# Kernel tuning notes

Hardware: AMD Instinct MI355X
Metric: run time of the kernel (lower is better)

## Reference

```python
import jax, jax.numpy as jnp
import numpy as np
from jax import lax

C, H, W, N = 128, 48, 48, 16
SHIFT_W = 1   # frozen value of p_3_1_1 (random.randint(-3,3) in original)
SHIFT_C = 1   # frozen value of p_11_0_1


def setup_inputs() -> dict:
    key = jax.random.key(0)
    k1, k2, k3, k4, k5 = jax.random.split(key, 5)
    x = jax.random.normal(k1, (N, C, H, W), dtype=jnp.float32)
    # p_5_w: trunc_normal std=0.02, shape (1,c,h,w)
    p5_w = 0.02 * jax.random.truncated_normal(k2, -2.0, 2.0, (1, C, H, W), dtype=jnp.float32)
    # p_6: 1x1 conv c->c, no bias -> weight (c, c)
    w6 = jax.random.normal(k3, (C, C), dtype=jnp.float32) / np.float32(np.sqrt(C))
    # p_8: Conv2d(1, c//2, (1,5), dilation=(1,3), padding=(0,6), bias=False)
    w8 = jax.random.normal(k4, (C // 2, 1, 1, 5), dtype=jnp.float32) / np.float32(np.sqrt(5))
    # p_10: 1x1 conv 3c/2 -> c, no bias
    w10 = jax.random.normal(k5, (C, 3 * C // 2), dtype=jnp.float32) / np.float32(np.sqrt(3 * C // 2))
    return {"x": x, "p5_w": p5_w, "w6": w6, "w8": w8, "w10": w10}


def _forward(x, p5_w, w6, w8, w10):
    n, c, h, w = x.shape
    hw = h * w
    inv_sqrt_c = np.float32(1.0 / np.sqrt(c))
    inv_sqrt_hw = np.float32(1.0 / np.sqrt(hw))

    t1 = x.max(axis=1)                                    # (n,h,w) channel max
    t2 = -x
    t4 = jnp.maximum(t2, jnp.roll(t2, SHIFT_W, axis=3))    # roll along width
    t5 = p5_w * t4
    t6 = jnp.einsum('oc,nchw->nohw', w6, t5)               # 1x1 conv p_6

    # score tensor t_7: (n, hw, hw)
    t7 = jnp.einsum('ncp,ncq->npq', t6.reshape(n, c, hw), x.reshape(n, c, hw)) * inv_sqrt_c

    # dilated 1x5 conv on channel-max map
    t8 = lax.conv_general_dilated(
        t1[:, None, :, :], w8, window_strides=(1, 1),
        padding=((0, 0), (6, 6)), rhs_dilation=(1, 3),
        dimension_numbers=('NCHW', 'OIHW', 'NCHW'))        # (n, c/2, h, w)

    # unfold kernel (3,1), dilation (2,1), padding (2,0): rows i-2, i, i+2
    pad = jnp.pad(t8, ((0, 0), (0, 0), (2, 2), (0, 0)))
    t9 = jnp.stack([pad[:, :, 2 * k:2 * k + h, :] for k in range(3)], axis=2)  # (n,c/2,3,h,w)

    t10 = jnp.einsum('oc,nchw->nohw', w10, t9.reshape(n, 3 * c // 2, h, w))   # 1x1 conv p_10
    t11 = jnp.roll(t10, SHIFT_C, axis=1)                   # roll along channels
    t12 = jnp.maximum(x, t11)

    # out[n,q,c] = sum_p t7[n,p,q] * t12[n,c,p]
    t13 = jnp.einsum('npq,ncp->nqc', t7, t12.reshape(n, c, hw)) * inv_sqrt_hw
    return t13.reshape(n, h, w, c).transpose(0, 3, 1, 2)   # (n,c,h,w)


def reference(x, p5_w, w6, w8, w10):
    return _forward(x, p5_w, w6, w8, w10)
```

## Files before the change

kernel.cpp:

```cpp
#include <hip/hip_runtime.h>
#include <cmath>

typedef short bf16x8 __attribute__((ext_vector_type(8)));
typedef short bf16x4 __attribute__((ext_vector_type(4)));
typedef float f32x4 __attribute__((ext_vector_type(4)));

namespace {
constexpr int kN   = 16;
constexpr int kC   = 128;
constexpr int kH   = 48;
constexpr int kW   = 48;
constexpr int kHW  = kH * kW;
constexpr int kK9  = 192;
constexpr int kNPC = 18;
constexpr int kPCH = kHW / kNPC;
constexpr int kLS  = 132;
constexpr int kPA  = 136;
}

__device__ __forceinline__ unsigned short f2b(float f) {
  unsigned u = __builtin_bit_cast(unsigned, f);
  u = (u + 0x7FFFu + ((u >> 16) & 1u)) >> 16;
  return (unsigned short)u;
}
__device__ __forceinline__ float b2f(unsigned short u) {
  return __builtin_bit_cast(float, ((unsigned)u) << 16);
}

__device__ __forceinline__ int tidx(int w, int c) {
  return w * kLS + (c ^ (((w >> 2) & 3) << 3));
}

__global__ __launch_bounds__(256)
void k_prep(const float* __restrict__ p5, const float* __restrict__ w6,
            const float* __restrict__ w10, const float* __restrict__ w8,
            float* __restrict__ p5T, unsigned short* __restrict__ w6b,
            float* __restrict__ Weff) {
  const int tid = threadIdx.x;
  const int bb = blockIdx.x;
  if (bb < 48) {
    __shared__ float Ls[kW * kLS];
    const int h = bb;
    for (int i = 0; i < 6; ++i) {
      const int idx = i * 256 + tid;
      const int c = idx / 12, s = idx % 12;
      const float4 v = *(const float4*)(p5 + (size_t)c * kHW + h * kW + s * 4);
      const int sw = (s & 3) << 3;
      Ls[(4 * s + 0) * kLS + (c ^ sw)] = v.x;
      Ls[(4 * s + 1) * kLS + (c ^ sw)] = v.y;
      Ls[(4 * s + 2) * kLS + (c ^ sw)] = v.z;
      Ls[(4 * s + 3) * kLS + (c ^ sw)] = v.w;
    }
    __syncthreads();
    for (int i = 0; i < 3; ++i) {
      const int idx = i * 256 + tid;
      const int w = idx >> 4, c = (idx & 15) * 8;
      const float* s = &Ls[tidx(w, c)];
      float4 a{s[0], s[1], s[2], s[3]}, b{s[4], s[5], s[6], s[7]};
      float* dst = p5T + ((size_t)(h * kW + w)) * kC + c;
      *(float4*)dst = a;
      *(float4*)(dst + 4) = b;
    }
  } else if (bb < 112) {
    const int i = (bb - 48) * 256 + tid;
    w6b[i] = f2b(w6[i]);
  } else {
    const int idx = (bb - 112) * 256 + tid;
    if (idx < kC * 15) {
      const int o = idx / 15, t = idx - o * 15;
      const int kk = t / 5, j = t - kk * 5;
      float s = 0.f;
#pragma unroll
      for (int c2 = 0; c2 < 64; ++c2)
        s = fmaf(w10[o * kK9 + 3 * c2 + kk], w8[c2 * 5 + j], s);
      Weff[idx] = s;
    }
  }
}

__global__ __launch_bounds__(256)
void k_xt5t6(const float* __restrict__ x, const float* __restrict__ p5T,
             const unsigned short* __restrict__ w6b,
             unsigned short* __restrict__ xT, unsigned short* __restrict__ xB,
             float* __restrict__ t1, unsigned short* __restrict__ t6) {
  __shared__ __align__(16) float Ls[kW * kLS];
  __shared__ __align__(16) unsigned short w6s[kC * kPA];
  __shared__ __align__(16) unsigned short t5s[kW * kPA];
  const int b = blockIdx.x;
  const int n = b / kH, h = b - n * kH;
  const int tid = threadIdx.x;
  const float* xrow = x + (size_t)n * kC * kHW + h * kW;
  unsigned short* xBrow = xB + (size_t)n * kC * kHW + h * kW;
  for (int i = 0; i < 6; ++i) {
    const int idx = i * 256 + tid;
    const int c = idx / 12, s = idx % 12;
    const float4 v = *(const float4*)(xrow + (size_t)c * kHW + s * 4);
    const int sw = (s & 3) << 3;
    Ls[(4 * s + 0) * kLS + (c ^ sw)] = v.x;
    Ls[(4 * s + 1) * kLS + (c ^ sw)] = v.y;
    Ls[(4 * s + 2) * kLS + (c ^ sw)] = v.z;
    Ls[(4 * s + 3) * kLS + (c ^ sw)] = v.w;
    bf16x4 xb4{(short)f2b(v.x), (short)f2b(v.y), (short)f2b(v.z), (short)f2b(v.w)};
    *(bf16x4*)(xBrow + (size_t)c * kHW + s * 4) = xb4;
  }
  for (int i = 0; i < 8; ++i) {
    const int f = i * 256 + tid;
    const int o = f >> 4, seg = (f & 15) * 8;
    *(bf16x8*)&w6s[o * kPA + seg] = *(const bf16x8*)(w6b + o * kC + seg);
  }
  __syncthreads();

  for (int i = 0; i < 3; ++i) {
    const int idx = i * 256 + tid;
    const int w = idx >> 4, c = (idx & 15) * 8;
    const int wp = (w == 0) ? (kW - 1) : (w - 1);
    const float* sv = &Ls[tidx(w, c)];
    const float* sp = &Ls[tidx(wp, c)];
    const int q = h * kW + w;
    const float* pv = p5T + (size_t)q * kC + c;

    unsigned short xb[8], tb[8];
    float m = -3.4e38f;
#pragma unroll
    for (int j = 0; j < 8; ++j) {
      const float xv = sv[j];
      const float t5 = pv[j] * fmaxf(-xv, -sp[j]);
      xb[j] = f2b(xv);
      tb[j] = f2b(t5);
      m = fmaxf(m, xv);
    }
    *(bf16x8*)(xT + ((size_t)n * kHW + q) * kC + c) = *(const bf16x8*)xb;
    *(bf16x8*)&t5s[w * kPA + c] = *(const bf16x8*)tb;
#pragma unroll
    for (int off = 1; off < 16; off <<= 1)
      m = fmaxf(m, __shfl_xor(m, off, 16));
    if ((tid & 15) == 0) t1[(size_t)n * kHW + q] = m;
  }
  __syncthreads();

  const int wv = tid >> 6, lane = tid & 63;
  const int lr = lane & 15, lk = (lane >> 4) * 8;
  f32x4 acc[2][3];
#pragma unroll
  for (int i = 0; i < 2; ++i)
#pragma unroll
    for (int j = 0; j < 3; ++j) acc[i][j] = f32x4{0.f, 0.f, 0.f, 0.f};
#pragma unroll
  for (int ks = 0; ks < kC; ks += 32) {
    bf16x8 a[2], bf[3];
#pragma unroll
    for (int mt = 0; mt < 2; ++mt)
      a[mt] = *(const bf16x8*)&w6s[(32 * wv + 16 * mt + lr) * kPA + ks + lk];
#pragma unroll
    for (int nt = 0; nt < 3; ++nt)
      bf[nt] = *(const bf16x8*)&t5s[(16 * nt + lr) * kPA + ks + lk];
#pragma unroll
    for (int mt = 0; mt < 2; ++mt)
#pragma unroll
      for (int nt = 0; nt < 3; ++nt)
        acc[mt][nt] = __builtin_amdgcn_mfma_f32_16x16x32_bf16(a[mt], bf[nt], acc[mt][nt], 0, 0, 0);
  }
#pragma unroll
  for (int mt = 0; mt < 2; ++mt)
#pragma unroll
    for (int nt = 0; nt < 3; ++nt) {
      const int q = h * kW + 16 * nt + lr;
#pragma unroll
      for (int r = 0; r < 4; ++r) {
        const int o = 32 * wv + 16 * mt + 4 * (lane >> 4) + r;
        t6[((size_t)n * kC + o) * kHW + q] = f2b(acc[mt][nt][r]);
      }
    }
}

__global__ __launch_bounds__(256)
void k_corr(const unsigned short* __restrict__ xB, const float* __restrict__ t1,
            const float* __restrict__ Weff, const unsigned short* __restrict__ t6,
            unsigned short* __restrict__ part) {
  __shared__ __align__(16) unsigned short t12s[kC * kPA];
  __shared__ __align__(16) unsigned short Bsf[kC * kPA];
  __shared__ __align__(16) float t1s[8 * 60];
  __shared__ float sW[kC][15];
  const int tid = threadIdx.x;
  const int n = blockIdx.y;
  const int chunk = blockIdx.x;
  const int p0 = chunk * kPCH;
  const int h_lo = p0 / kW;
  const unsigned short* Bg = t6 + (size_t)n * kC * kHW + p0;

  for (int i = tid; i < 8 * 60; i += 256) {
    const int r = i / 60, cc = i - r * 60;
    const int hh = h_lo - 2 + r, ww = cc - 6;
    t1s[i] = (hh >= 0 && hh < kH && ww >= 0 && ww < kW) ? t1[n * kHW + hh * kW + ww] : 0.f;
  }
  for (int i = tid; i < kC * 15; i += 256) {
    const int c = i / 15, t = i - c * 15;
    sW[c][t] = Weff[((c - 1) & (kC - 1)) * 15 + t];
  }
#pragma unroll
  for (int i = 0; i < 8; ++i) {
    const int f = i * 256 + tid;
    const int c = f >> 4, seg = (f & 15) * 8;
    *(bf16x8*)&Bsf[c * kPA + seg] = *(const bf16x8*)(Bg + (size_t)c * kHW + seg);
  }
  __syncthreads();

  const unsigned short* xn = xB + (size_t)n * kC * kHW;
  for (int it = 0; it < 8; ++it) {
    const int idx = it * 256 + tid;
    const int c = idx >> 4, p = (idx & 15) * 8;
    const int q = p0 + p;
    const int h = q / kW, w0 = q - h * kW;
    const int r0 = h - h_lo;
    float tap[3][20];
#pragma unroll
    for (int kk = 0; kk < 3; ++kk) {
      const float* src = &t1s[(r0 + 2 * kk) * 60 + w0];
#pragma unroll
      for (int j4 = 0; j4 < 5; ++j4) {
        const float4 v = *(const float4*)(src + 4 * j4);
        tap[kk][4 * j4 + 0] = v.x; tap[kk][4 * j4 + 1] = v.y;
        tap[kk][4 * j4 + 2] = v.z; tap[kk][4 * j4 + 3] = v.w;
      }
    }
    float wr[15];
#pragma unroll
    for (int t = 0; t < 15; ++t) wr[t] = sW[c][t];
    const bf16x8 xv8 = *(const bf16x8*)(xn + (size_t)c * kHW + q);
    unsigned short o16[8];
#pragma unroll
    for (int dp = 0; dp < 8; ++dp) {
      float acc = 0.f;
#pragma unroll
      for (int kk = 0; kk < 3; ++kk)
#pragma unroll
        for (int j = 0; j < 5; ++j)
          acc = fmaf(wr[kk * 5 + j], tap[kk][3 * j + dp], acc);
      o16[dp] = f2b(fmaxf(b2f((unsigned short)xv8[dp]), acc));
    }
    *(bf16x8*)&t12s[c * kPA + p] = *(const bf16x8*)o16;
  }
  __syncthreads();

  const int wv = tid >> 6, lane = tid & 63;
  const int lr = lane & 15, lk = (lane >> 4) * 8;
  const int wr2 = (wv >> 1) * 64, wc2 = (wv & 1) * 64;
  f32x4 acc[4][4];
#pragma unroll
  for (int i = 0; i < 4; ++i)
#pragma unroll
    for (int j = 0; j < 4; ++j) acc[i][j] = f32x4{0.f, 0.f, 0.f, 0.f};

#pragma unroll
  for (int ks = 0; ks < kPCH; ks += 32) {
    bf16x8 a[4], bv[4];
#pragma unroll
    for (int i = 0; i < 4; ++i) {
      a[i]  = *(const bf16x8*)&t12s[(wr2 + 16 * i + lr) * kPA + ks + lk];
      bv[i] = *(const bf16x8*)&Bsf[(wc2 + 16 * i + lr) * kPA + ks + lk];
    }
#pragma unroll
    for (int i = 0; i < 4; ++i)
#pragma unroll
      for (int j = 0; j < 4; ++j)
        acc[i][j] = __builtin_amdgcn_mfma_f32_16x16x32_bf16(a[i], bv[j], acc[i][j], 0, 0, 0);
  }

  unsigned short* dst = part + ((size_t)chunk * kN + n) * (kC * kC);
#pragma unroll
  for (int i = 0; i < 4; ++i)
#pragma unroll
    for (int j = 0; j < 4; ++j)
#pragma unroll
      for (int r = 0; r < 4; ++r)
        dst[(wr2 + 16 * i + 4 * (lane >> 4) + r) * kC + wc2 + 16 * j + lr] = f2b(acc[i][j][r]);
}

__global__ __launch_bounds__(256)
void k_redM(const unsigned short* __restrict__ part, unsigned short* __restrict__ M) {
  const int bid = blockIdx.x;
  const int j = bid >> 4, n = bid & 15;
  const int r0 = (j * 256 + threadIdx.x) * 8;
  float acc[8];
#pragma unroll
  for (int e = 0; e < 8; ++e) acc[e] = 0.f;
#pragma unroll
  for (int ch = 0; ch < kNPC; ++ch) {
    const bf16x8 v = *(const bf16x8*)(part + (((size_t)ch * kN + n) << 14) + r0);
#pragma unroll
    for (int e = 0; e < 8; ++e) acc[e] += b2f((unsigned short)v[e]);
  }
  unsigned short o16[8];
#pragma unroll
  for (int e = 0; e < 8; ++e) o16[e] = f2b(acc[e]);
  *(bf16x8*)(M + ((size_t)n << 14) + r0) = *(const bf16x8*)o16;
}

__global__ __launch_bounds__(256)
void k_out(const unsigned short* __restrict__ A, const unsigned short* __restrict__ B,
           float* __restrict__ Out, float scale) {
  constexpr int K = 128;
  __shared__ __align__(16) unsigned short As[kC * kPA];
  __shared__ __align__(16) unsigned short Bs[64 * kPA];
  const int tid = threadIdx.x;
  const int n = blockIdx.y;
  const int qbase = blockIdx.x * 64;
  const unsigned short* Ag = A + (size_t)n * kC * K;
  const unsigned short* Bg = B + ((size_t)n * kHW + qbase) * K;

  {
    const int m = tid >> 1, hf = tid & 1;
    const unsigned short* src = Ag + (size_t)m * K + hf * 64;
    unsigned short* dst = &As[m * kPA + hf * 64];
#pragma unroll
    for (int i = 0; i < 8; ++i)
      *(bf16x8*)(dst + 8 * i) = *(const bf16x8*)(src + 8 * i);
  }
#pragma unroll
  for (int i = 0; i < 4; ++i) {
    const int f = i * 256 + tid;
    const int q = f >> 4, seg = (f & 15) * 8;
    *(bf16x8*)&Bs[q * kPA + seg] = *(const bf16x8*)(Bg + (size_t)q * K + seg);
  }
  __syncthreads();

  const int wv = tid >> 6, lane = tid & 63;
  const int lr = lane & 15, lk = (lane >> 4) * 8;

  f32x4 acc[2][4];
#pragma unroll
  for (int i = 0; i < 2; ++i)
#pragma unroll
    for (int j = 0; j < 4; ++j) acc[i][j] = f32x4{0.f, 0.f, 0.f, 0.f};

#pragma unroll
  for (int ks = 0; ks < K; ks += 32) {
    bf16x8 a[2], b[4];
#pragma unroll
    for (int mt = 0; mt < 2; ++mt)
      a[mt] = *(const bf16x8*)&As[(32 * wv + 16 * mt + lr) * kPA + ks + lk];
#pragma unroll
    for (int nt = 0; nt < 4; ++nt)
      b[nt] = *(const bf16x8*)&Bs[(16 * nt + lr) * kPA + ks + lk];
#pragma unroll
    for (int mt = 0; mt < 2; ++mt)
#pragma unroll
      for (int nt = 0; nt < 4; ++nt)
        acc[mt][nt] = __builtin_amdgcn_mfma_f32_16x16x32_bf16(
            a[mt], b[nt], acc[mt][nt], 0, 0, 0);
  }

#pragma unroll
  for (int mt = 0; mt < 2; ++mt)
#pragma unroll
    for (int nt = 0; nt < 4; ++nt) {
      const int q = qbase + 16 * nt + lr;
#pragma unroll
      for (int r = 0; r < 4; ++r) {
        const int m = 32 * wv + 16 * mt + 4 * (lane >> 4) + r;
        Out[((size_t)n * kC + m) * kHW + q] = scale * acc[mt][nt][r];
      }
    }
}

extern "C" void kernel_launch(void* const* d_in, const int* in_sizes, int n_in,
                              void* d_out, int out_size, void* d_ws, size_t ws_size,
                              hipStream_t stream) {
  const float* x   = (const float*)d_in[0];
  const float* p5  = (const float*)d_in[1];
  const float* w6  = (const float*)d_in[2];
  const float* w8  = (const float*)d_in[3];
  const float* w10 = (const float*)d_in[4];
  float* out = (float*)d_out;

  char* ws = (char*)d_ws;
  unsigned short* xT   = (unsigned short*)(ws);
  unsigned short* t6b  = (unsigned short*)(ws + 9437184);
  unsigned short* part = (unsigned short*)(ws + 18874368);
  unsigned short* xB   = (unsigned short*)(ws + 28311552);
  unsigned short* Mb   = (unsigned short*)(ws + 37748736);
  float*          t1b  = (float*)(ws + 38273024);
  unsigned short* w6b  = (unsigned short*)(ws + 38420480);
  float*          Weff = (float*)(ws + 38453248);
  float*          p5T  = (float*)(ws + 38460928);

  const float scale = 1.0f / (sqrtf((float)kC) * sqrtf((float)kHW));

  k_prep<<<120, 256, 0, stream>>>(p5, w6, w10, w8, p5T, w6b, Weff);
  k_xt5t6<<<kN * kH, 256, 0, stream>>>(x, p5T, w6b, xT, xB, t1b, t6b);
  k_corr<<<dim3(kNPC, kN), 256, 0, stream>>>(xB, t1b, Weff, t6b, part);
  k_redM<<<8 * kN, 256, 0, stream>>>(part, Mb);
  k_out<<<dim3(kHW / 64, kN), 256, 0, stream>>>(Mb, xT, out, scale);
}
```

Measured before the change: 48.71 us.

## Fuse partial reduction into k_corr via last-block atomic counter; drop LDS staging

```diff
diff --git a/kernel.cpp b/kernel.cpp
--- a/kernel.cpp
+++ b/kernel.cpp
@@ -35,7 +35,7 @@
 void k_prep(const float* __restrict__ p5, const float* __restrict__ w6,
             const float* __restrict__ w10, const float* __restrict__ w8,
             float* __restrict__ p5T, unsigned short* __restrict__ w6b,
-            float* __restrict__ Weff) {
+            float* __restrict__ Weff, int* __restrict__ cnt) {
   const int tid = threadIdx.x;
   const int bb = blockIdx.x;
   if (bb < 48) {
@@ -75,6 +75,7 @@
         s = fmaf(w10[o * kK9 + 3 * c2 + kk], w8[c2 * 5 + j], s);
       Weff[idx] = s;
     }
+    if (bb == 119 && tid < kN) cnt[tid] = 0;
   }
 }
 
@@ -84,7 +85,6 @@
              unsigned short* __restrict__ xT, unsigned short* __restrict__ xB,
              float* __restrict__ t1, unsigned short* __restrict__ t6) {
   __shared__ __align__(16) float Ls[kW * kLS];
-  __shared__ __align__(16) unsigned short w6s[kC * kPA];
   __shared__ __align__(16) unsigned short t5s[kW * kPA];
   const int b = blockIdx.x;
   const int n = b / kH, h = b - n * kH;
@@ -103,11 +103,6 @@
     bf16x4 xb4{(short)f2b(v.x), (short)f2b(v.y), (short)f2b(v.z), (short)f2b(v.w)};
     *(bf16x4*)(xBrow + (size_t)c * kHW + s * 4) = xb4;
   }
-  for (int i = 0; i < 8; ++i) {
-    const int f = i * 256 + tid;
-    const int o = f >> 4, seg = (f & 15) * 8;
-    *(bf16x8*)&w6s[o * kPA + seg] = *(const bf16x8*)(w6b + o * kC + seg);
-  }
   __syncthreads();
 
   for (int i = 0; i < 3; ++i) {
@@ -150,7 +145,7 @@
     bf16x8 a[2], bf[3];
 #pragma unroll
     for (int mt = 0; mt < 2; ++mt)
-      a[mt] = *(const bf16x8*)&w6s[(32 * wv + 16 * mt + lr) * kPA + ks + lk];
+      a[mt] = *(const bf16x8*)(w6b + (size_t)(32 * wv + 16 * mt + lr) * kC + ks + lk);
 #pragma unroll
     for (int nt = 0; nt < 3; ++nt)
       bf[nt] = *(const bf16x8*)&t5s[(16 * nt + lr) * kPA + ks + lk];
@@ -176,7 +171,8 @@
 __global__ __launch_bounds__(256)
 void k_corr(const unsigned short* __restrict__ xB, const float* __restrict__ t1,
             const float* __restrict__ Weff, const unsigned short* __restrict__ t6,
-            unsigned short* __restrict__ part) {
+            unsigned short* __restrict__ part, unsigned short* __restrict__ M,
+            int* __restrict__ cnt) {
   __shared__ __align__(16) unsigned short t12s[kC * kPA];
   __shared__ __align__(16) unsigned short Bsf[kC * kPA];
   __shared__ __align__(16) float t1s[8 * 60];
@@ -274,33 +270,37 @@
 #pragma unroll
       for (int r = 0; r < 4; ++r)
         dst[(wr2 + 16 * i + 4 * (lane >> 4) + r) * kC + wc2 + 16 * j + lr] = f2b(acc[i][j][r]);
-}
-
-__global__ __launch_bounds__(256)
-void k_redM(const unsigned short* __restrict__ part, unsigned short* __restrict__ M) {
-  const int bid = blockIdx.x;
-  const int j = bid >> 4, n = bid & 15;
-  const int r0 = (j * 256 + threadIdx.x) * 8;
-  float acc[8];
-#pragma unroll
-  for (int e = 0; e < 8; ++e) acc[e] = 0.f;
-#pragma unroll
-  for (int ch = 0; ch < kNPC; ++ch) {
-    const bf16x8 v = *(const bf16x8*)(part + (((size_t)ch * kN + n) << 14) + r0);
-#pragma unroll
-    for (int e = 0; e < 8; ++e) acc[e] += b2f((unsigned short)v[e]);
-  }
-  unsigned short o16[8];
-#pragma unroll
-  for (int e = 0; e < 8; ++e) o16[e] = f2b(acc[e]);
-  *(bf16x8*)(M + ((size_t)n << 14) + r0) = *(const bf16x8*)o16;
+
+  __threadfence();
+  __shared__ int isLast;
+  if (tid == 0) isLast = (atomicAdd(&cnt[n], 1) == kNPC - 1);
+  __syncthreads();
+  if (isLast) {
+    __threadfence();
+#pragma unroll
+    for (int jb = 0; jb < 8; ++jb) {
+      const int r0 = (jb * 256 + tid) * 8;
+      float acc8[8];
+#pragma unroll
+      for (int e = 0; e < 8; ++e) acc8[e] = 0.f;
+#pragma unroll
+      for (int ch = 0; ch < kNPC; ++ch) {
+        const bf16x8 v = *(const bf16x8*)(part + (((size_t)ch * kN + n) << 14) + r0);
+#pragma unroll
+        for (int e = 0; e < 8; ++e) acc8[e] += b2f((unsigned short)v[e]);
+      }
+      unsigned short o16[8];
+#pragma unroll
+      for (int e = 0; e < 8; ++e) o16[e] = f2b(acc8[e]);
+      *(bf16x8*)(M + ((size_t)n << 14) + r0) = *(const bf16x8*)o16;
+    }
+  }
 }
 
 __global__ __launch_bounds__(256)
 void k_out(const unsigned short* __restrict__ A, const unsigned short* __restrict__ B,
            float* __restrict__ Out, float scale) {
   constexpr int K = 128;
-  __shared__ __align__(16) unsigned short As[kC * kPA];
   __shared__ __align__(16) unsigned short Bs[64 * kPA];
   const int tid = threadIdx.x;
   const int n = blockIdx.y;
@@ -308,14 +308,6 @@
   const unsigned short* Ag = A + (size_t)n * kC * K;
   const unsigned short* Bg = B + ((size_t)n * kHW + qbase) * K;
 
-  {
-    const int m = tid >> 1, hf = tid & 1;
-    const unsigned short* src = Ag + (size_t)m * K + hf * 64;
-    unsigned short* dst = &As[m * kPA + hf * 64];
-#pragma unroll
-    for (int i = 0; i < 8; ++i)
-      *(bf16x8*)(dst + 8 * i) = *(const bf16x8*)(src + 8 * i);
-  }
 #pragma unroll
   for (int i = 0; i < 4; ++i) {
     const int f = i * 256 + tid;
@@ -338,7 +330,7 @@
     bf16x8 a[2], b[4];
 #pragma unroll
     for (int mt = 0; mt < 2; ++mt)
-      a[mt] = *(const bf16x8*)&As[(32 * wv + 16 * mt + lr) * kPA + ks + lk];
+      a[mt] = *(const bf16x8*)(Ag + (size_t)(32 * wv + 16 * mt + lr) * K + ks + lk);
 #pragma unroll
     for (int nt = 0; nt < 4; ++nt)
       b[nt] = *(const bf16x8*)&Bs[(16 * nt + lr) * kPA + ks + lk];
@@ -383,12 +375,12 @@
   unsigned short* w6b  = (unsigned short*)(ws + 38420480);
   float*          Weff = (float*)(ws + 38453248);
   float*          p5T  = (float*)(ws + 38460928);
+  int*            cnt  = (int*)(ws + 39640576);
 
   const float scale = 1.0f / (sqrtf((float)kC) * sqrtf((float)kHW));
 
-  k_prep<<<120, 256, 0, stream>>>(p5, w6, w10, w8, p5T, w6b, Weff);
+  k_prep<<<120, 256, 0, stream>>>(p5, w6, w10, w8, p5T, w6b, Weff, cnt);
   k_xt5t6<<<kN * kH, 256, 0, stream>>>(x, p5T, w6b, xT, xB, t1b, t6b);
-  k_corr<<<dim3(kNPC, kN), 256, 0, stream>>>(xB, t1b, Weff, t6b, part);
-  k_redM<<<8 * kN, 256, 0, stream>>>(part, Mb);
+  k_corr<<<dim3(kNPC, kN), 256, 0, stream>>>(xB, t1b, Weff, t6b, part, Mb, cnt);
   k_out<<<dim3(kHW / 64, kN), 256, 0, stream>>>(Mb, xT, out, scale);
 }
```

After: 100.3 us. +105.8%, slower.
